# Performance work log

Measured on AMD Instinct MI355X. Metric: run time of the kernel, lower is better.

The kernel has to match this reference:

```python
import jax, jax.numpy as jnp
import numpy as np

B, N, D, H = 4, 1024, 512, 8
DH = D // H  # per-head dim for V and for each of the two Q/K halves
LAM = 0.5


def setup_inputs() -> dict:
    key = jax.random.key(0)
    ks = jax.random.split(key, 7)
    s = 0.02
    return {
        "x": jax.random.normal(ks[0], (B, N, D), dtype=jnp.float32),
        "Wq": jax.random.normal(ks[1], (D, 2 * D), dtype=jnp.float32) * s,
        "bq": jax.random.normal(ks[2], (2 * D,), dtype=jnp.float32) * s,
        "Wk": jax.random.normal(ks[3], (D, 2 * D), dtype=jnp.float32) * s,
        "bk": jax.random.normal(ks[4], (2 * D,), dtype=jnp.float32) * s,
        "Wv": jax.random.normal(ks[5], (D, D), dtype=jnp.float32) * s,
        "bv": jax.random.normal(ks[6], (D,), dtype=jnp.float32) * s,
    }


def reference(x, Wq, bq, Wk, bk, Wv, bv):
    b, n, d = x.shape
    q = (x @ Wq + bq).reshape(b, n, H, 2 * DH).transpose(0, 2, 1, 3)  # [B,H,N,2*DH]
    k = (x @ Wk + bk).reshape(b, n, H, 2 * DH).transpose(0, 2, 1, 3)
    v = (x @ Wv + bv).reshape(b, n, H, DH).transpose(0, 2, 1, 3)      # [B,H,N,DH]
    q1, q2 = q[..., :DH], q[..., DH:]
    k1, k2 = k[..., :DH], k[..., DH:]
    scale = 1.0 / jnp.sqrt(jnp.float32(DH))
    a1 = jax.nn.softmax(jnp.einsum("bhqd,bhkd->bhqk", q1, k1) * scale, axis=-1)
    a2 = jax.nn.softmax(jnp.einsum("bhqd,bhkd->bhqk", q2, k2) * scale, axis=-1)
    attn = a1 - LAM * a2                                              # [B,H,N,N]
    out = jnp.einsum("bhqk,bhkd->bhqd", attn, v)                      # [B,H,N,DH]
    return out.transpose(0, 2, 1, 3).reshape(b, n, d)
```

## Files before the change

### kernel.cpp

```cpp
#include <hip/hip_runtime.h>
#include <hip/hip_bf16.h>

typedef unsigned short u16;
typedef short s16x8 __attribute__((ext_vector_type(8)));
typedef float f32x4 __attribute__((ext_vector_type(4)));

__device__ inline u16 f2bf(float f) {
  union { float f; unsigned int u; } v; v.f = f;
  unsigned int r = v.u + 0x7fffu + ((v.u >> 16) & 1u);
  return (u16)(r >> 16);
}

__device__ __forceinline__ void g2lds16(const u16* g, u16* l) {
  __builtin_amdgcn_global_load_lds((const __attribute__((address_space(1))) void*)g,
                                   (__attribute__((address_space(3))) void*)l, 16, 0, 0);
}

__global__ __launch_bounds__(256) void cast_x_kernel(const float* __restrict__ x,
                                                     u16* __restrict__ xb) {
  int i = (blockIdx.x * 256 + threadIdx.x) * 8;
  float4 a = *(const float4*)(x + i);
  float4 b = *(const float4*)(x + i + 4);
  s16x8 o;
  o[0] = (short)f2bf(a.x); o[1] = (short)f2bf(a.y);
  o[2] = (short)f2bf(a.z); o[3] = (short)f2bf(a.w);
  o[4] = (short)f2bf(b.x); o[5] = (short)f2bf(b.y);
  o[6] = (short)f2bf(b.z); o[7] = (short)f2bf(b.w);
  *(s16x8*)(xb + i) = o;
}

__global__ __launch_bounds__(256) void transpose_cast_w(const float* __restrict__ src, int C,
                                                        int rowoff, u16* __restrict__ wt) {
  __shared__ float tile[64][65];
  int j0 = blockIdx.x * 64, k0 = blockIdx.y * 64;
  int tx = threadIdx.x % 64, ty4 = threadIdx.x / 64;
#pragma unroll
  for (int p = 0; p < 16; ++p) {
    int r = p * 4 + ty4;
    tile[r][tx] = src[(size_t)(k0 + r) * C + j0 + tx];
  }
  __syncthreads();
#pragma unroll
  for (int p = 0; p < 16; ++p) {
    int r = p * 4 + ty4;
    wt[(size_t)(rowoff + j0 + r) * 512 + k0 + tx] = f2bf(tile[tx][r]);
  }
}

__global__ __launch_bounds__(256, 2) void gemm_qkv(const u16* __restrict__ xb, const u16* __restrict__ wt,
                                                   const float* __restrict__ bq, const float* __restrict__ bk,
                                                   const float* __restrict__ bv,
                                                   u16* __restrict__ qa, u16* __restrict__ ka,
                                                   u16* __restrict__ va) {
  __shared__ __align__(16) u16 As[128 * 64];
  __shared__ __align__(16) u16 Bs[128 * 64];
  int m0 = blockIdx.x * 128, j0 = blockIdx.y * 128;
  int tid = threadIdx.x;
  int w = tid >> 6, lane = tid & 63, quad = lane >> 4, l16 = lane & 15;
  int wr = (w >> 1) * 64, wc = (w & 1) * 64;

  int srow[4], scol[4], sbase[4];
#pragma unroll
  for (int it = 0; it < 4; ++it) {
    int s = it * 256 + tid;
    srow[it] = s >> 3;
    scol[it] = (s & 7) ^ ((s >> 3) & 7);
    sbase[it] = (s & ~63) * 8;
  }

  f32x4 acc[4][4];
#pragma unroll
  for (int i = 0; i < 4; ++i)
#pragma unroll
    for (int j = 0; j < 4; ++j)
#pragma unroll
      for (int r = 0; r < 4; ++r) acc[i][j][r] = 0.f;

  for (int kk = 0; kk < 8; ++kk) {
    int k0 = kk * 64;
    __syncthreads();
#pragma unroll
    for (int it = 0; it < 4; ++it) {
      g2lds16(xb + (size_t)(m0 + srow[it]) * 512 + k0 + scol[it] * 8, &As[sbase[it]]);
      g2lds16(wt + (size_t)(j0 + srow[it]) * 512 + k0 + scol[it] * 8, &Bs[sbase[it]]);
    }
    __syncthreads();
#pragma unroll
    for (int kb = 0; kb < 2; ++kb) {
      s16x8 af[4], bfr[4];
#pragma unroll
      for (int rb = 0; rb < 4; ++rb) {
        int row = wr + rb * 16 + l16;
        af[rb] = *(const s16x8*)(&As[row * 64 + (((kb * 4 + quad) ^ (row & 7)) * 8)]);
      }
#pragma unroll
      for (int cb = 0; cb < 4; ++cb) {
        int row = wc + cb * 16 + l16;
        bfr[cb] = *(const s16x8*)(&Bs[row * 64 + (((kb * 4 + quad) ^ (row & 7)) * 8)]);
      }
#pragma unroll
      for (int rb = 0; rb < 4; ++rb)
#pragma unroll
        for (int cb = 0; cb < 4; ++cb)
          acc[rb][cb] = __builtin_amdgcn_mfma_f32_16x16x32_bf16(af[rb], bfr[cb], acc[rb][cb], 0, 0, 0);
    }
  }

#pragma unroll
  for (int cb = 0; cb < 4; ++cb) {
    int j = j0 + wc + cb * 16 + l16;
    float bias = (j < 1024) ? bq[j] : (j < 2048) ? bk[j - 1024] : bv[j - 2048];
#pragma unroll
    for (int rb = 0; rb < 4; ++rb) {
#pragma unroll
      for (int r = 0; r < 4; ++r) {
        int m = m0 + wr + rb * 16 + quad * 4 + r;
        int bidx = m >> 10, n = m & 1023;
        u16 o = f2bf(acc[rb][cb][r] + bias);
        if (j < 1024) {
          int h = j >> 7, r2 = j & 127;
          qa[((size_t)((bidx * 8 + h) * 1024 + n)) * 128 + r2] = o;
        } else if (j < 2048) {
          int jj = j - 1024, h = jj >> 7, r2 = jj & 127;
          ka[((size_t)((bidx * 8 + h) * 1024 + n)) * 128 + r2] = o;
        } else {
          int jj = j - 2048, h = jj >> 6, d = jj & 63;
          va[((size_t)((bidx * 8 + h) * 64 + d)) * 1024 + n] = o;
        }
      }
    }
  }
}

__global__ __launch_bounds__(256, 2) void attn_kernel(const u16* __restrict__ qa, const u16* __restrict__ ka,
                                                      const u16* __restrict__ va, float* __restrict__ out) {
  __shared__ __align__(16) u16 Ks[2][64 * 128];
  __shared__ __align__(16) u16 Vs[2][64 * 64];
  __shared__ __align__(16) u16 Ps[2][64 * 72];
  int bh = blockIdx.x, b = bh >> 3, h = bh & 7;
  int q0 = blockIdx.y * 64;
  int tid = threadIdx.x, w = tid >> 6, lane = tid & 63, quad = lane >> 4, l16 = lane & 15;

  const u16* qrow = qa + (size_t)(bh * 1024 + q0 + w * 16 + l16) * 128;
  s16x8 qf[2][2];
  qf[0][0] = *(const s16x8*)(qrow + quad * 8);
  qf[0][1] = *(const s16x8*)(qrow + 32 + quad * 8);
  qf[1][0] = *(const s16x8*)(qrow + 64 + quad * 8);
  qf[1][1] = *(const s16x8*)(qrow + 96 + quad * 8);

  f32x4 O1[5], O2[5];
#pragma unroll
  for (int i = 0; i < 5; ++i)
#pragma unroll
    for (int r = 0; r < 4; ++r) { O1[i][r] = 0.f; O2[i][r] = 0.f; }

  s16x8 onesf;
#pragma unroll
  for (int i = 0; i < 8; ++i) onesf[i] = (l16 == 0) ? (short)0x3F80 : (short)0;

  int krow[4], kcol[4], kbse[4];
#pragma unroll
  for (int it = 0; it < 4; ++it) {
    int s = it * 256 + tid;
    krow[it] = s >> 4; kcol[it] = (s & 15) ^ ((s >> 4) & 7); kbse[it] = (s & ~63) * 8;
  }
  int vrow[2], vcol[2], vbse[2];
#pragma unroll
  for (int it = 0; it < 2; ++it) {
    int s = it * 256 + tid;
    vrow[it] = s >> 3; vcol[it] = (s & 7) ^ ((s >> 3) & 7); vbse[it] = (s & ~63) * 8;
  }
  const u16* kgbase = ka + (size_t)bh * 1024 * 128;
  const u16* vgbase = va + (size_t)bh * 64 * 1024;

  auto stage = [&](int kt, int bufi) {
    int n0 = kt * 64;
#pragma unroll
    for (int it = 0; it < 4; ++it)
      g2lds16(kgbase + (size_t)(n0 + krow[it]) * 128 + kcol[it] * 8, &Ks[bufi][kbse[it]]);
#pragma unroll
    for (int it = 0; it < 2; ++it)
      g2lds16(vgbase + (size_t)vrow[it] * 1024 + n0 + vcol[it] * 8, &Vs[bufi][vbse[it]]);
  };

  stage(0, 0);
  __syncthreads();

  for (int kt = 0; kt < 16; ++kt) {
    int cur = kt & 1;
    if (kt < 15) stage(kt + 1, cur ^ 1);

    s16x8 vf[4][2];
#pragma unroll
    for (int ct = 0; ct < 4; ++ct)
#pragma unroll
      for (int kb = 0; kb < 2; ++kb) {
        int row = ct * 16 + l16;
        vf[ct][kb] = *(const s16x8*)(&Vs[cur][row * 64 + (((kb * 4 + quad) ^ (row & 7)) * 8)]);
      }

#pragma unroll
    for (int hh = 0; hh < 2; ++hh) {
#pragma unroll
      for (int nt = 0; nt < 4; ++nt) {
        f32x4 sv; sv[0] = sv[1] = sv[2] = sv[3] = 0.f;
#pragma unroll
        for (int kb = 0; kb < 2; ++kb) {
          int row = nt * 16 + l16;
          s16x8 kf = *(const s16x8*)(&Ks[cur][row * 128 + (((hh * 8 + kb * 4 + quad) ^ (row & 7)) * 8)]);
          sv = __builtin_amdgcn_mfma_f32_16x16x32_bf16(qf[hh][kb], kf, sv, 0, 0, 0);
        }
#pragma unroll
        for (int r = 0; r < 4; ++r)
          Ps[hh][(w * 16 + quad * 4 + r) * 72 + nt * 16 + l16] = f2bf(__expf(sv[r] * 0.125f));
      }
    }
    asm volatile("s_waitcnt lgkmcnt(0)" ::: "memory");
    s16x8 pf[2][2];
#pragma unroll
    for (int hh = 0; hh < 2; ++hh) {
      pf[hh][0] = *(const s16x8*)(&Ps[hh][(w * 16 + l16) * 72 + quad * 8]);
      pf[hh][1] = *(const s16x8*)(&Ps[hh][(w * 16 + l16) * 72 + 32 + quad * 8]);
    }
#pragma unroll
    for (int ct = 0; ct < 5; ++ct) {
      s16x8 b0 = (ct < 4) ? vf[ct][0] : onesf;
      s16x8 b1 = (ct < 4) ? vf[ct][1] : onesf;
      O1[ct] = __builtin_amdgcn_mfma_f32_16x16x32_bf16(pf[0][0], b0, O1[ct], 0, 0, 0);
      O1[ct] = __builtin_amdgcn_mfma_f32_16x16x32_bf16(pf[0][1], b1, O1[ct], 0, 0, 0);
      O2[ct] = __builtin_amdgcn_mfma_f32_16x16x32_bf16(pf[1][0], b0, O2[ct], 0, 0, 0);
      O2[ct] = __builtin_amdgcn_mfma_f32_16x16x32_bf16(pf[1][1], b1, O2[ct], 0, 0, 0);
    }
    __syncthreads();
  }

  float inv1[4], inv2[4];
#pragma unroll
  for (int r = 0; r < 4; ++r) {
    float l1 = __shfl(O1[4][r], lane & 48, 64);
    float l2 = __shfl(O2[4][r], lane & 48, 64);
    inv1[r] = 1.0f / l1;
    inv2[r] = 1.0f / l2;
  }
  int nb = q0 + w * 16 + quad * 4;
#pragma unroll
  for (int ct = 0; ct < 4; ++ct)
#pragma unroll
    for (int r = 0; r < 4; ++r) {
      float val = O1[ct][r] * inv1[r] - 0.5f * O2[ct][r] * inv2[r];
      out[(size_t)(b * 1024 + nb + r) * 512 + h * 64 + ct * 16 + l16] = val;
    }
}

extern "C" void kernel_launch(void* const* d_in, const int* in_sizes, int n_in,
                              void* d_out, int out_size, void* d_ws, size_t ws_size,
                              hipStream_t stream) {
  (void)in_sizes; (void)n_in; (void)out_size; (void)ws_size;
  const float* x  = (const float*)d_in[0];
  const float* Wq = (const float*)d_in[1];
  const float* bq = (const float*)d_in[2];
  const float* Wk = (const float*)d_in[3];
  const float* bk = (const float*)d_in[4];
  const float* Wv = (const float*)d_in[5];
  const float* bv = (const float*)d_in[6];
  float* out = (float*)d_out;

  char* ws = (char*)d_ws;
  u16* xb = (u16*)(ws);
  u16* wt = (u16*)(ws + 4194304);
  u16* qa = (u16*)(ws + 6815744);
  u16* ka = (u16*)(ws + 15204352);
  u16* va = (u16*)(ws + 23592960);

  cast_x_kernel<<<1024, 256, 0, stream>>>(x, xb);
  transpose_cast_w<<<dim3(16, 8), 256, 0, stream>>>(Wq, 1024, 0, wt);
  transpose_cast_w<<<dim3(16, 8), 256, 0, stream>>>(Wk, 1024, 1024, wt);
  transpose_cast_w<<<dim3(8, 8), 256, 0, stream>>>(Wv, 512, 2048, wt);
  gemm_qkv<<<dim3(32, 20), 256, 0, stream>>>(xb, wt, bq, bk, bv, qa, ka, va);
  attn_kernel<<<dim3(32, 16), 256, 0, stream>>>(qa, ka, va, out);
}
```

Measured before the change: 138.0 us.

## Software-pipeline attention PV with next QK, merge weight transpose launches

Restructures the attention loop so the P·V MFMAs for the previous tile run interleaved with the QK MFMAs of the current tile. This uses a triple-buffered V in LDS and drops the mid-iteration LDS wait. QK now computes the transposed score tile, so each lane can pack four bf16 probabilities with v_cvt_pk_bf16 and store them as one 8-byte LDS write, using exp2 with a folded scale. The three weight transpose-cast launches are merged into one. Extra LDS for the third V buffer and more live registers may reduce occupancy.

```diff
diff --git a/kernel.cpp b/kernel.cpp
--- a/kernel.cpp
+++ b/kernel.cpp
@@ -2,6 +2,7 @@
 #include <hip/hip_bf16.h>
 
 typedef unsigned short u16;
+typedef unsigned int u32;
 typedef short s16x8 __attribute__((ext_vector_type(8)));
 typedef float f32x4 __attribute__((ext_vector_type(4)));
 
@@ -9,6 +10,12 @@
   union { float f; unsigned int u; } v; v.f = f;
   unsigned int r = v.u + 0x7fffu + ((v.u >> 16) & 1u);
   return (u16)(r >> 16);
+}
+
+__device__ __forceinline__ u32 cvt_pk_bf16(float lo, float hi) {
+  u32 r;
+  asm("v_cvt_pk_bf16_f32 %0, %1, %2" : "=v"(r) : "v"(lo), "v"(hi));
+  return r;
 }
 
 __device__ __forceinline__ void g2lds16(const u16* g, u16* l) {
@@ -29,10 +36,17 @@
   *(s16x8*)(xb + i) = o;
 }
 
-__global__ __launch_bounds__(256) void transpose_cast_w(const float* __restrict__ src, int C,
-                                                        int rowoff, u16* __restrict__ wt) {
+__global__ __launch_bounds__(256) void transpose_cast_w_all(const float* __restrict__ Wq,
+                                                            const float* __restrict__ Wk,
+                                                            const float* __restrict__ Wv,
+                                                            u16* __restrict__ wt) {
   __shared__ float tile[64][65];
-  int j0 = blockIdx.x * 64, k0 = blockIdx.y * 64;
+  int jg = blockIdx.x * 64;
+  const float* src; int C, j0;
+  if (jg < 1024)      { src = Wq; C = 1024; j0 = jg; }
+  else if (jg < 2048) { src = Wk; C = 1024; j0 = jg - 1024; }
+  else                { src = Wv; C = 512;  j0 = jg - 2048; }
+  int k0 = blockIdx.y * 64;
   int tx = threadIdx.x % 64, ty4 = threadIdx.x / 64;
 #pragma unroll
   for (int p = 0; p < 16; ++p) {
@@ -43,7 +57,7 @@
 #pragma unroll
   for (int p = 0; p < 16; ++p) {
     int r = p * 4 + ty4;
-    wt[(size_t)(rowoff + j0 + r) * 512 + k0 + tx] = f2bf(tile[tx][r]);
+    wt[(size_t)(jg + r) * 512 + k0 + tx] = f2bf(tile[tx][r]);
   }
 }
 
@@ -135,7 +149,7 @@
 __global__ __launch_bounds__(256, 2) void attn_kernel(const u16* __restrict__ qa, const u16* __restrict__ ka,
                                                       const u16* __restrict__ va, float* __restrict__ out) {
   __shared__ __align__(16) u16 Ks[2][64 * 128];
-  __shared__ __align__(16) u16 Vs[2][64 * 64];
+  __shared__ __align__(16) u16 Vs[3][64 * 64];
   __shared__ __align__(16) u16 Ps[2][64 * 72];
   int bh = blockIdx.x, b = bh >> 3, h = bh & 7;
   int q0 = blockIdx.y * 64;
@@ -173,55 +187,107 @@
   const u16* kgbase = ka + (size_t)bh * 1024 * 128;
   const u16* vgbase = va + (size_t)bh * 64 * 1024;
 
-  auto stage = [&](int kt, int bufi) {
-    int n0 = kt * 64;
+  auto stageK = [&](int n0, u16* Kd) {
 #pragma unroll
     for (int it = 0; it < 4; ++it)
-      g2lds16(kgbase + (size_t)(n0 + krow[it]) * 128 + kcol[it] * 8, &Ks[bufi][kbse[it]]);
+      g2lds16(kgbase + (size_t)(n0 + krow[it]) * 128 + kcol[it] * 8, Kd + kbse[it]);
+  };
+  auto stageV = [&](int n0, u16* Vd) {
 #pragma unroll
     for (int it = 0; it < 2; ++it)
-      g2lds16(vgbase + (size_t)vrow[it] * 1024 + n0 + vcol[it] * 8, &Vs[bufi][vbse[it]]);
+      g2lds16(vgbase + (size_t)vrow[it] * 1024 + n0 + vcol[it] * 8, Vd + vbse[it]);
   };
 
-  stage(0, 0);
+  stageK(0, &Ks[0][0]);
+  stageV(0, &Vs[0][0]);
   __syncthreads();
 
+  int prow = (w * 16 + l16) * 72;
+  s16x8 pf[2][2];
+  int cv = 0;
+
   for (int kt = 0; kt < 16; ++kt) {
-    int cur = kt & 1;
-    if (kt < 15) stage(kt + 1, cur ^ 1);
-
+    int kc = kt & 1;
+    int nv = (cv == 2) ? 0 : cv + 1;
+    int pv = (cv == 0) ? 2 : cv - 1;
+    if (kt < 15) { stageK((kt + 1) * 64, &Ks[kc ^ 1][0]); stageV((kt + 1) * 64, &Vs[nv][0]); }
+
+    if (kt > 0) {
+#pragma unroll
+      for (int hh = 0; hh < 2; ++hh) {
+        pf[hh][0] = *(const s16x8*)(&Ps[hh][prow + quad * 8]);
+        pf[hh][1] = *(const s16x8*)(&Ps[hh][prow + 32 + quad * 8]);
+      }
+    }
+
+    const u16* KsC = &Ks[kc][0];
+    f32x4 sv[2][4];
+#pragma unroll
+    for (int hh = 0; hh < 2; ++hh)
+#pragma unroll
+      for (int nt = 0; nt < 4; ++nt) {
+        f32x4 s; s[0] = s[1] = s[2] = s[3] = 0.f;
+#pragma unroll
+        for (int kb = 0; kb < 2; ++kb) {
+          int row = nt * 16 + l16;
+          s16x8 kf = *(const s16x8*)(&KsC[row * 128 + (((hh * 8 + kb * 4 + quad) ^ (row & 7)) * 8)]);
+          s = __builtin_amdgcn_mfma_f32_16x16x32_bf16(kf, qf[hh][kb], s, 0, 0, 0);
+        }
+        sv[hh][nt] = s;
+      }
+
+    if (kt > 0) {
+      const u16* VsP = &Vs[pv][0];
+      s16x8 vf[4][2];
+#pragma unroll
+      for (int ct = 0; ct < 4; ++ct)
+#pragma unroll
+        for (int kb = 0; kb < 2; ++kb) {
+          int row = ct * 16 + l16;
+          vf[ct][kb] = *(const s16x8*)(&VsP[row * 64 + (((kb * 4 + quad) ^ (row & 7)) * 8)]);
+        }
+#pragma unroll
+      for (int ct = 0; ct < 5; ++ct) {
+        s16x8 b0 = (ct < 4) ? vf[ct][0] : onesf;
+        s16x8 b1 = (ct < 4) ? vf[ct][1] : onesf;
+        O1[ct] = __builtin_amdgcn_mfma_f32_16x16x32_bf16(pf[0][0], b0, O1[ct], 0, 0, 0);
+        O1[ct] = __builtin_amdgcn_mfma_f32_16x16x32_bf16(pf[0][1], b1, O1[ct], 0, 0, 0);
+        O2[ct] = __builtin_amdgcn_mfma_f32_16x16x32_bf16(pf[1][0], b0, O2[ct], 0, 0, 0);
+        O2[ct] = __builtin_amdgcn_mfma_f32_16x16x32_bf16(pf[1][1], b1, O2[ct], 0, 0, 0);
+      }
+    }
+
+#pragma unroll
+    for (int hh = 0; hh < 2; ++hh)
+#pragma unroll
+      for (int nt = 0; nt < 4; ++nt) {
+        float e0 = __builtin_exp2f(sv[hh][nt][0] * 0.18033688f);
+        float e1 = __builtin_exp2f(sv[hh][nt][1] * 0.18033688f);
+        float e2 = __builtin_exp2f(sv[hh][nt][2] * 0.18033688f);
+        float e3 = __builtin_exp2f(sv[hh][nt][3] * 0.18033688f);
+        uint2 pw; pw.x = cvt_pk_bf16(e0, e1); pw.y = cvt_pk_bf16(e2, e3);
+        *(uint2*)(&Ps[hh][prow + nt * 16 + quad * 4]) = pw;
+      }
+
+    cv = nv;
+    __syncthreads();
+  }
+
+  {
+#pragma unroll
+    for (int hh = 0; hh < 2; ++hh) {
+      pf[hh][0] = *(const s16x8*)(&Ps[hh][prow + quad * 8]);
+      pf[hh][1] = *(const s16x8*)(&Ps[hh][prow + 32 + quad * 8]);
+    }
+    const u16* VsP = &Vs[0][0];
     s16x8 vf[4][2];
 #pragma unroll
     for (int ct = 0; ct < 4; ++ct)
 #pragma unroll
       for (int kb = 0; kb < 2; ++kb) {
         int row = ct * 16 + l16;
-        vf[ct][kb] = *(const s16x8*)(&Vs[cur][row * 64 + (((kb * 4 + quad) ^ (row & 7)) * 8)]);
-      }
-
-#pragma unroll
-    for (int hh = 0; hh < 2; ++hh) {
-#pragma unroll
-      for (int nt = 0; nt < 4; ++nt) {
-        f32x4 sv; sv[0] = sv[1] = sv[2] = sv[3] = 0.f;
-#pragma unroll
-        for (int kb = 0; kb < 2; ++kb) {
-          int row = nt * 16 + l16;
-          s16x8 kf = *(const s16x8*)(&Ks[cur][row * 128 + (((hh * 8 + kb * 4 + quad) ^ (row & 7)) * 8)]);
-          sv = __builtin_amdgcn_mfma_f32_16x16x32_bf16(qf[hh][kb], kf, sv, 0, 0, 0);
-        }
-#pragma unroll
-        for (int r = 0; r < 4; ++r)
-          Ps[hh][(w * 16 + quad * 4 + r) * 72 + nt * 16 + l16] = f2bf(__expf(sv[r] * 0.125f));
-      }
-    }
-    asm volatile("s_waitcnt lgkmcnt(0)" ::: "memory");
-    s16x8 pf[2][2];
-#pragma unroll
-    for (int hh = 0; hh < 2; ++hh) {
-      pf[hh][0] = *(const s16x8*)(&Ps[hh][(w * 16 + l16) * 72 + quad * 8]);
-      pf[hh][1] = *(const s16x8*)(&Ps[hh][(w * 16 + l16) * 72 + 32 + quad * 8]);
-    }
+        vf[ct][kb] = *(const s16x8*)(&VsP[row * 64 + (((kb * 4 + quad) ^ (row & 7)) * 8)]);
+      }
 #pragma unroll
     for (int ct = 0; ct < 5; ++ct) {
       s16x8 b0 = (ct < 4) ? vf[ct][0] : onesf;
@@ -231,7 +297,6 @@
       O2[ct] = __builtin_amdgcn_mfma_f32_16x16x32_bf16(pf[1][0], b0, O2[ct], 0, 0, 0);
       O2[ct] = __builtin_amdgcn_mfma_f32_16x16x32_bf16(pf[1][1], b1, O2[ct], 0, 0, 0);
     }
-    __syncthreads();
   }
 
   float inv1[4], inv2[4];
@@ -273,9 +338,7 @@
   u16* va = (u16*)(ws + 23592960);
 
   cast_x_kernel<<<1024, 256, 0, stream>>>(x, xb);
-  transpose_cast_w<<<dim3(16, 8), 256, 0, stream>>>(Wq, 1024, 0, wt);
-  transpose_cast_w<<<dim3(16, 8), 256, 0, stream>>>(Wk, 1024, 1024, wt);
-  transpose_cast_w<<<dim3(8, 8), 256, 0, stream>>>(Wv, 512, 2048, wt);
+  transpose_cast_w_all<<<dim3(40, 8), 256, 0, stream>>>(Wq, Wk, Wv, wt);
   gemm_qkv<<<dim3(32, 20), 256, 0, stream>>>(xb, wt, bq, bk, bv, qa, ka, va);
   attn_kernel<<<dim3(32, 16), 256, 0, stream>>>(qa, ka, va, out);
 }
```

Result: faster. 134.8 us (-2.3%).
